# Kernel optimization log

Measured on AMD Instinct MI355X. Metric: run time of the kernel, lower is better.

The kernel has to match this reference:

```python
import jax, jax.numpy as jnp
import numpy as np

DIM = 128      # input node feature dim
GS = 64        # SAGEConv output dim
AF = 32        # additional (ir_score) feature dim
NB = 2         # nb_classes
G = 8192       # num_graphs in batch
NPG = 16       # nodes per graph
N = G * NPG    # total nodes = 131072
E = 2097152    # total edges (avg degree 16)


def setup_inputs() -> dict:
    key = jax.random.key(0)
    ks = jax.random.split(key, 10)

    def w(k, shape, fan_in):
        return jax.random.normal(k, shape, jnp.float32) / np.sqrt(fan_in)

    return {
        "x": jax.random.normal(ks[0], (N, DIM), jnp.float32),
        "edge_index": jax.random.randint(ks[1], (2, E), 0, N),
        "set_indices": jax.random.randint(ks[2], (G, 2), 0, NPG),
        "batch_ids": jnp.repeat(jnp.arange(G), NPG),  # sorted graph ids, PyG style
        "ir_score": jax.random.uniform(ks[3], (G, AF), jnp.float32),
        "W_l": w(ks[4], (DIM, GS), DIM),
        "b_l": jnp.zeros((GS,), jnp.float32),
        "W_r": w(ks[5], (DIM, GS), DIM),
        "W_ir": w(ks[6], (AF, 2 * GS), AF),
        "b_ir": jnp.zeros((2 * GS,), jnp.float32),
        "W1": w(ks[7], ((2 * GS) * (2 * GS), 200), (2 * GS) * (2 * GS)),
        "b1": jnp.zeros((200,), jnp.float32),
        "W2": w(ks[8], (200, NB), 200),
        "b2": jnp.zeros((NB,), jnp.float32),
    }


def reference(x, edge_index, set_indices, batch_ids, ir_score,
              W_l, b_l, W_r, W_ir, b_ir, W1, b1, W2, b2):
    n = x.shape[0]
    src, dst = edge_index[0], edge_index[1]

    # SAGEConv (mean aggregation): out = lin_l(mean_{j in N(i)} x_j) + lin_r(x_i)
    agg = jax.ops.segment_sum(x[src], dst, num_segments=n)           # [N, DIM]
    deg = jax.ops.segment_sum(jnp.ones((src.shape[0],), x.dtype), dst, num_segments=n)
    mean = agg / jnp.maximum(deg, 1.0)[:, None]
    h = jax.nn.relu(mean @ W_l + b_l + x @ W_r)                      # [N, GS]

    # per-graph node counts -> index bases (cumsum), then global pair indices
    g = set_indices.shape[0]
    num_nodes = jax.ops.segment_sum(jnp.ones((n,), jnp.float32), batch_ids, num_segments=g)
    csum = jnp.cumsum(num_nodes.astype(jnp.int64))
    index_bases = jnp.concatenate([jnp.zeros((1,), jnp.int64), csum[:-1]])
    sib = index_bases[:, None] + set_indices                         # [G, 2]

    pair = h[sib].reshape(g, 2 * GS)                                 # gather + flatten

    # fusion: relu(linear(ir_score)) then per-graph outer product
    S = jax.nn.relu(ir_score @ W_ir + b_ir)                          # [G, 2*GS]
    outer = jnp.einsum('gi,gj->gij', pair, S).reshape(g, -1)         # [G, (2GS)^2]

    # decode MLP
    z = jax.nn.relu(outer @ W1 + b1)                                 # [G, 200]
    logits = z @ W2 + b2                                             # [G, NB]
    return logits
```

## Files before the change

kernel.cpp:

```cpp
#include <hip/hip_runtime.h>

#define NN   131072
#define GG   8192
#define EE   2097152
#define KBIG 16384
#define NPAD 224
#define NSPLIT 8
#define NSEL  16384
#define SBUCK 256
#define SUBC  4
#define SCAPS 336
#define SCAPT (SUBC*SCAPS)

typedef _Float16 half_t;
typedef __attribute__((ext_vector_type(8))) _Float16 half8;
typedef __attribute__((ext_vector_type(4))) float floatx4;

__device__ inline floatx4 mfma16(half8 a, half8 b, floatx4 c) {
  return __builtin_amdgcn_mfma_f32_16x16x32_f16(a, b, c, 0, 0, 0);
}

__global__ void prep_w(const float* __restrict__ Wl, const float* __restrict__ Wr,
                       half_t* __restrict__ Wt) {
  int idx = blockIdx.x * blockDim.x + threadIdx.x;
  int n = idx >> 7, k = idx & 127;
  float v = (n < 64) ? Wl[k * 64 + n] : Wr[k * 64 + (n - 64)];
  Wt[n * 128 + k] = (half_t)v;
}
__global__ void prep_w1p(const float* __restrict__ W1, half_t* __restrict__ W1p) {
  int idx = blockIdx.x * blockDim.x + threadIdx.x;
  int lane = idx & 63;
  int t = idx >> 6;
  int nt = t % 14; t /= 14;
  int jj = t & 1;  t >>= 1;
  int i  = t & 15; t >>= 4;
  int ph = t & 1;  t >>= 1;
  int split = t;
  int n = nt * 16 + (lane & 15);
  int k0 = split * 2048 + i * 128 + ph * 64 + jj * 32 + (lane >> 4) * 8;
  half8 v;
#pragma unroll
  for (int e = 0; e < 8; e++)
    v[e] = (half_t)((n < 200) ? W1[(size_t)(k0 + e) * 200 + n] : 0.f);
  *(half8*)(W1p + (size_t)idx * 8) = v;
}

__global__ void set_slots(const int* __restrict__ set_idx, int* __restrict__ nodemap,
                          int* __restrict__ slot_node) {
  int idx = blockIdx.x * blockDim.x + threadIdx.x;
  int g = idx >> 1, which = idx & 1;
  int node = g * 16 + set_idx[g * 2 + which];
  slot_node[idx] = node;
  nodemap[node] = idx;
}

__global__ void filter_scatter(const int* __restrict__ src, const int* __restrict__ dst,
                               const int* __restrict__ nodemap,
                               int* __restrict__ scnt, unsigned int* __restrict__ sbuf) {
  int e = blockIdx.x * blockDim.x + threadIdx.x;
  int d = dst[e];
  int slot = nodemap[d];
  if (slot >= 0) {
    int b = slot >> 6;
    int sub = blockIdx.x & (SUBC - 1);
    int pos = atomicAdd(&scnt[(b * SUBC + sub) * 16], 1);
    if (pos < SCAPS)
      sbuf[(size_t)(b * SUBC + sub) * SCAPS + pos] =
          (unsigned int)src[e] | ((unsigned int)(slot & 63) << 17);
  }
}

__global__ __launch_bounds__(256) void y_gemm(const float* __restrict__ x,
                                              const half_t* __restrict__ WtG,
                                              half_t* __restrict__ y16) {
  __shared__ half_t wlds[64 * 128];
  __shared__ half_t ybuf[64 * 72];
  int tid = threadIdx.x, w = tid >> 6, lane = tid & 63;
  int m = lane & 15, q = lane >> 4, kc = q * 8;
#pragma unroll
  for (int it = 0; it < 4; it++) {
    int cb = (it * 4 + w) * 64;
    const half_t* g = WtG + ((size_t)cb + lane) * 8;
    half_t* l = wlds + (size_t)cb * 8;
    __builtin_amdgcn_global_load_lds((const __attribute__((address_space(1))) uint32_t*)g,
                                     (__attribute__((address_space(3))) uint32_t*)l, 16, 0, 0);
  }
  int node0 = blockIdx.x * 64 + w * 16;
  float4 xu[4][2];
#pragma unroll
  for (int step = 0; step < 4; step++) {
    const float* xp = x + (size_t)(node0 + m) * 128 + step * 32 + kc;
    xu[step][0] = *(const float4*)xp;
    xu[step][1] = *(const float4*)(xp + 4);
  }
  __syncthreads();
  floatx4 acc[4];
#pragma unroll
  for (int nt = 0; nt < 4; nt++) acc[nt] = (floatx4){0.f, 0.f, 0.f, 0.f};
#pragma unroll
  for (int step = 0; step < 4; step++) {
    float4 u0 = xu[step][0], u1 = xu[step][1];
    half8 av = {(half_t)u0.x, (half_t)u0.y, (half_t)u0.z, (half_t)u0.w,
                (half_t)u1.x, (half_t)u1.y, (half_t)u1.z, (half_t)u1.w};
    int k0 = step * 32 + kc;
#pragma unroll
    for (int nt = 0; nt < 4; nt++) {
      half8 bv = *(const half8*)(wlds + (nt * 16 + m) * 128 + k0);
      acc[nt] = mfma16(av, bv, acc[nt]);
    }
  }
#pragma unroll
  for (int nt = 0; nt < 4; nt++)
#pragma unroll
    for (int r = 0; r < 4; r++)
      ybuf[(w * 16 + q * 4 + r) * 72 + nt * 16 + m] = (half_t)acc[nt][r];
  __syncthreads();
#pragma unroll
  for (int c = tid; c < 512; c += 256) {
    int row = c >> 3, co = (c & 7) * 8;
    *(half8*)(y16 + (size_t)(blockIdx.x * 64 + row) * 64 + co) =
        *(const half8*)(ybuf + row * 72 + co);
  }
}

__global__ __launch_bounds__(256) void r_slots(const float* __restrict__ x,
                                               const half_t* __restrict__ WtG,
                                               const float* __restrict__ b_l,
                                               const int* __restrict__ slot_node,
                                               half_t* __restrict__ r_slot) {
  int tid = threadIdx.x, w = tid >> 6, lane = tid & 63;
  int m = lane & 15, q = lane >> 4, kc = q * 8;
  int s0 = blockIdx.x * 64 + w * 16;
  int node = slot_node[s0 + m];
  floatx4 acc[4];
#pragma unroll
  for (int nt = 0; nt < 4; nt++) acc[nt] = (floatx4){0.f, 0.f, 0.f, 0.f};
#pragma unroll
  for (int step = 0; step < 4; step++) {
    int k0 = step * 32 + kc;
    const float* xp = x + (size_t)node * 128 + k0;
    float4 u0 = *(const float4*)xp;
    float4 u1 = *(const float4*)(xp + 4);
    half8 av = {(half_t)u0.x, (half_t)u0.y, (half_t)u0.z, (half_t)u0.w,
                (half_t)u1.x, (half_t)u1.y, (half_t)u1.z, (half_t)u1.w};
#pragma unroll
    for (int nt = 0; nt < 4; nt++) {
      half8 bv = *(const half8*)(WtG + (size_t)(64 + nt * 16 + m) * 128 + k0);
      acc[nt] = mfma16(av, bv, acc[nt]);
    }
  }
#pragma unroll
  for (int nt = 0; nt < 4; nt++) {
    int n = nt * 16 + m;
    float bias = b_l[n];
#pragma unroll
    for (int r = 0; r < 4; r++) {
      int s = s0 + q * 4 + r;
      r_slot[(size_t)s * 64 + n] = (half_t)(acc[nt][r] + bias);
    }
  }
}

__global__ __launch_bounds__(256) void slot_agg(const unsigned int* __restrict__ sbuf,
                                                const int* __restrict__ scnt,
                                                const half_t* __restrict__ y16,
                                                const half_t* __restrict__ r_slot,
                                                half_t* __restrict__ h_slot) {
  __shared__ int sorted[SCAPT];
  __shared__ int hist[64];
  __shared__ int base[64];
  __shared__ int start[65];
  int b = blockIdx.x, tid = threadIdx.x;
  if (tid < 64) hist[tid] = 0;
  __syncthreads();
  unsigned int myedge[2 * SUBC];
  int mycnt = 0;
#pragma unroll
  for (int sub = 0; sub < SUBC; sub++) {
    int n = scnt[(b * SUBC + sub) * 16]; if (n > SCAPS) n = SCAPS;
    const unsigned int* eb = sbuf + (size_t)(b * SUBC + sub) * SCAPS;
    for (int e = tid; e < n; e += 256) {
      unsigned int pk = eb[e];
      myedge[mycnt++] = pk;
      atomicAdd(&hist[pk >> 17], 1);
    }
  }
  __syncthreads();
  if (tid < 64) {
    int v = hist[tid];
    int sum = v;
#pragma unroll
    for (int off = 1; off < 64; off <<= 1) {
      int u = __shfl_up(sum, off);
      if (tid >= off) sum += u;
    }
    start[tid] = sum - v;
    base[tid]  = sum - v;
    if (tid == 63) start[64] = sum;
  }
  __syncthreads();
  for (int i = 0; i < mycnt; i++) {
    unsigned int pk = myedge[i];
    int pos = atomicAdd(&base[pk >> 17], 1);
    sorted[pos] = (int)(pk & 0x1FFFF);
  }
  __syncthreads();
  int s = tid >> 2, p = tid & 3;
  int e0 = start[s], e1 = start[s + 1];
  float acc[16];
#pragma unroll
  for (int j = 0; j < 16; j++) acc[j] = 0.f;
  int e = e0;
  for (; e + 2 <= e1; e += 2) {
    int s0 = sorted[e], s1 = sorted[e + 1];
    const half8* p0 = (const half8*)(y16 + (size_t)s0 * 64 + p * 16);
    const half8* p1 = (const half8*)(y16 + (size_t)s1 * 64 + p * 16);
    half8 a0 = p0[0], c0 = p0[1], a1 = p1[0], c1 = p1[1];
#pragma unroll
    for (int j = 0; j < 8; j++) {
      acc[j]     += (float)a0[j] + (float)a1[j];
      acc[8 + j] += (float)c0[j] + (float)c1[j];
    }
  }
  if (e < e1) {
    int s0 = sorted[e];
    const half8* p0 = (const half8*)(y16 + (size_t)s0 * 64 + p * 16);
    half8 a0 = p0[0], c0 = p0[1];
#pragma unroll
    for (int j = 0; j < 8; j++) { acc[j] += (float)a0[j]; acc[8 + j] += (float)c0[j]; }
  }
  int slot = b * 64 + s;
  float inv = 1.0f / fmaxf((float)(e1 - e0), 1.0f);
  const half8* rr = (const half8*)(r_slot + (size_t)slot * 64 + p * 16);
  half8 r0 = rr[0], r1 = rr[1];
  half8 o0, o1;
#pragma unroll
  for (int j = 0; j < 8; j++) {
    o0[j] = (half_t)fmaxf(acc[j] * inv + (float)r0[j], 0.f);
    o1[j] = (half_t)fmaxf(acc[8 + j] * inv + (float)r1[j], 0.f);
  }
  half8* hp = (half8*)(h_slot + (size_t)slot * 64 + p * 16);
  hp[0] = o0;
  hp[1] = o1;
}

__global__ void s_pair_kernel(const float* __restrict__ ir, const float* __restrict__ W_ir,
                              const float* __restrict__ b_ir, half_t* __restrict__ S16,
                              const half_t* __restrict__ h_slot,
                              const int* __restrict__ nodemap,
                              const int* __restrict__ set_idx, half_t* __restrict__ pair16) {
  int idx = blockIdx.x * blockDim.x + threadIdx.x;
  int g = idx >> 7, o = idx & 127;
  const float* irow = ir + g * 32;
  float sv = b_ir[o];
#pragma unroll
  for (int a = 0; a < 32; a++) sv += irow[a] * W_ir[a * 128 + o];
  S16[idx] = (half_t)fmaxf(sv, 0.f);
  int which = o >> 6, c = o & 63;
  int node = g * 16 + set_idx[g * 2 + which];
  int slot = nodemap[node];
  pair16[idx] = h_slot[(size_t)slot * 64 + c];
}

__global__ __launch_bounds__(256, 2) void biggemm(const half_t* __restrict__ pair16,
                                                  const half_t* __restrict__ S16,
                                                  const half_t* __restrict__ W1p,
                                                  float* __restrict__ zpart) {
  __shared__ __align__(16) half_t bbuf[2][28 * 512];
  __shared__ half_t pls[16][128];
  int bx = blockIdx.x;
  int mt = bx >> 3, split = bx & 7;
  int g0 = mt * 128;
  int tid = threadIdx.x, w = tid >> 6, lane = tid & 63;
  int wm = w >> 1, wn = w & 1;
  int m = lane & 15, q = lane >> 4, kc = q * 8;
  int ntb = wn * 7;

  auto stage = [&](int s, int buf) {
#pragma unroll
    for (int ff = 0; ff < 7; ff++) {
      int f = ff * 4 + w;
      const half_t* gsrc = W1p + (((size_t)(split * 32 + s) * 28) + f) * 512 + lane * 8;
      half_t* ldst = &bbuf[buf][f * 512];
      __builtin_amdgcn_global_load_lds((const __attribute__((address_space(1))) uint32_t*)gsrc,
                                       (__attribute__((address_space(3))) uint32_t*)ldst, 16, 0, 0);
    }
  };

  {
    int row = tid & 127, sel = tid >> 7;
    half8 pa = *(const half8*)(pair16 + (size_t)(g0 + row) * 128 + split * 16 + sel * 8);
#pragma unroll
    for (int j = 0; j < 8; j++) pls[sel * 8 + j][row] = pa[j];
  }
  __syncthreads();

  stage(0, 0);
  stage(1, 1);

  floatx4 acc[4][7];
#pragma unroll
  for (int sb = 0; sb < 4; sb++)
#pragma unroll
    for (int t = 0; t < 7; t++) acc[sb][t] = (floatx4){0.f, 0.f, 0.f, 0.f};

  half8 sf[4][2];
#pragma unroll
  for (int ph = 0; ph < 2; ph++) {
#pragma unroll
    for (int sub = 0; sub < 4; sub++) {
      int grow = g0 + wm * 64 + sub * 16 + m;
#pragma unroll
      for (int j2 = 0; j2 < 2; j2++)
        sf[sub][j2] = *(const half8*)(S16 + (size_t)grow * 128 + ph * 64 + j2 * 32 + kc);
    }
#pragma unroll
    for (int i = 0; i < 16; i++) {
      const int s = ph * 16 + i;
      const int cur = s & 1;
      if (ph == 1 && i == 15) {
        asm volatile("s_waitcnt vmcnt(0)" ::: "memory");
      } else {
        asm volatile("s_waitcnt vmcnt(7)" ::: "memory");
      }
      __builtin_amdgcn_sched_barrier(0);
      __builtin_amdgcn_s_barrier();
      __builtin_amdgcn_sched_barrier(0);

      half_t p0 = pls[i][wm * 64 + 0 * 16 + m];
      half_t p1 = pls[i][wm * 64 + 1 * 16 + m];
      half_t p2 = pls[i][wm * 64 + 2 * 16 + m];
      half_t p3 = pls[i][wm * 64 + 3 * 16 + m];
      const half_t* bb = bbuf[cur];
#pragma unroll
      for (int jj = 0; jj < 2; jj++) {
        half8 a0 = sf[0][jj] * p0;
        half8 a1 = sf[1][jj] * p1;
        half8 a2 = sf[2][jj] * p2;
        half8 a3 = sf[3][jj] * p3;
#pragma unroll
        for (int t = 0; t < 7; t++) {
          half8 bv = *(const half8*)(bb + (jj * 14 + ntb + t) * 512 + lane * 8);
          acc[0][t] = mfma16(a0, bv, acc[0][t]);
          acc[1][t] = mfma16(a1, bv, acc[1][t]);
          acc[2][t] = mfma16(a2, bv, acc[2][t]);
          acc[3][t] = mfma16(a3, bv, acc[3][t]);
        }
      }

      if (s < 30) {
        __builtin_amdgcn_sched_barrier(0);
        __builtin_amdgcn_s_barrier();
        __builtin_amdgcn_sched_barrier(0);
        stage(s + 2, cur);
      }
    }
  }

#pragma unroll
  for (int sub = 0; sub < 4; sub++)
#pragma unroll
    for (int t = 0; t < 7; t++)
#pragma unroll
      for (int r = 0; r < 4; r++) {
        int row = g0 + wm * 64 + sub * 16 + q * 4 + r;
        zpart[((size_t)split * GG + row) * NPAD + (ntb + t) * 16 + m] = acc[sub][t][r];
      }
}

__global__ __launch_bounds__(256) void reduce_mlp(const float* __restrict__ zpart,
                                                  const float* __restrict__ b1,
                                                  const float* __restrict__ W2,
                                                  const float* __restrict__ b2,
                                                  float* __restrict__ out) {
  int tid = threadIdx.x;
  int w = tid >> 6, lane = tid & 63;
  int g = blockIdx.x * 4 + w;
  float p0 = 0.f, p1 = 0.f;
#pragma unroll
  for (int qq = 0; qq < 4; qq++) {
    int c = qq * 64 + lane;
    if (c < 200) {
      float z = 0.f;
#pragma unroll
      for (int sp = 0; sp < NSPLIT; sp++)
        z += zpart[((size_t)sp * GG + g) * NPAD + c];
      z += b1[c];
      z = fmaxf(z, 0.f);
      p0 += z * W2[c * 2];
      p1 += z * W2[c * 2 + 1];
    }
  }
#pragma unroll
  for (int off = 32; off; off >>= 1) {
    p0 += __shfl_down(p0, off);
    p1 += __shfl_down(p1, off);
  }
  if (lane == 0) {
    out[g * 2] = p0 + b2[0];
    out[g * 2 + 1] = p1 + b2[1];
  }
}

extern "C" void kernel_launch(void* const* d_in, const int* in_sizes, int n_in,
                              void* d_out, int out_size, void* d_ws, size_t ws_size,
                              hipStream_t stream) {
  const float* x     = (const float*)d_in[0];
  const int*   ei    = (const int*)d_in[1];
  const int*   setix = (const int*)d_in[2];
  const float* ir    = (const float*)d_in[4];
  const float* W_l   = (const float*)d_in[5];
  const float* b_l   = (const float*)d_in[6];
  const float* W_r   = (const float*)d_in[7];
  const float* W_ir  = (const float*)d_in[8];
  const float* b_ir  = (const float*)d_in[9];
  const float* W1    = (const float*)d_in[10];
  const float* b1    = (const float*)d_in[11];
  const float* W2    = (const float*)d_in[12];
  const float* b2    = (const float*)d_in[13];
  float* out = (float*)d_out;

  char* ws = (char*)d_ws;
  size_t off = 0;
  auto alloc = [&](size_t bytes) -> void* {
    void* p = ws + off;
    off = (off + bytes + 255) & ~(size_t)255;
    return p;
  };
  size_t pool_start = off;
  int* nodemap   = (int*)alloc((size_t)NN * 4);
  int* slot_node = (int*)alloc((size_t)NSEL * 4);
  int* scnt      = (int*)alloc((size_t)SBUCK * SUBC * 16 * 4);
  unsigned int* sbuf = (unsigned int*)alloc((size_t)SBUCK * SUBC * SCAPS * 4);
  half_t* y16    = (half_t*)alloc((size_t)NN * 64 * 2);
  half_t* r_slot = (half_t*)alloc((size_t)NSEL * 64 * 2);
  half_t* h_slot = (half_t*)alloc((size_t)NSEL * 64 * 2);
  float* zpart = (float*)(ws + pool_start);
  {
    size_t zend = pool_start + (((size_t)NSPLIT * GG * NPAD * 4 + 255) & ~(size_t)255);
    if (off < zend) off = zend;
  }
  half_t* Wt     = (half_t*)alloc(128 * 128 * 2);
  half_t* W1p    = (half_t*)alloc((size_t)NPAD * KBIG * 2);
  half_t* S16    = (half_t*)alloc((size_t)GG * 128 * 2);
  half_t* pair16 = (half_t*)alloc((size_t)GG * 128 * 2);
  (void)ws_size; (void)in_sizes; (void)n_in; (void)out_size;

  const int* esrc = ei;
  const int* edst = ei + EE;

  hipMemsetAsync(nodemap, 0xFF, (size_t)NN * 4, stream);
  hipMemsetAsync(scnt, 0, (size_t)SBUCK * SUBC * 16 * 4, stream);

  prep_w<<<(128 * 128) / 256, 256, 0, stream>>>(W_l, W_r, Wt);
  prep_w1p<<<(NPAD * KBIG / 8) / 256, 256, 0, stream>>>(W1, W1p);

  set_slots<<<NSEL / 256, 256, 0, stream>>>(setix, nodemap, slot_node);
  filter_scatter<<<EE / 256, 256, 0, stream>>>(esrc, edst, nodemap, scnt, sbuf);

  y_gemm<<<NN / 64, 256, 0, stream>>>(x, Wt, y16);
  r_slots<<<NSEL / 64, 256, 0, stream>>>(x, Wt, b_l, slot_node, r_slot);
  slot_agg<<<SBUCK, 256, 0, stream>>>(sbuf, scnt, y16, r_slot, h_slot);

  s_pair_kernel<<<(GG * 128) / 256, 256, 0, stream>>>(ir, W_ir, b_ir, S16, h_slot, nodemap, setix, pair16);

  biggemm<<<(GG / 128) * NSPLIT, 256, 0, stream>>>(pair16, S16, W1p, zpart);
  reduce_mlp<<<GG / 4, 256, 0, stream>>>(zpart, b1, W2, b2, out);
}
```

Measured before the change: 263.7 us.

## Fuse prep and mid kernels, replace nodemap lookup with direct set-index test

Merges the weight-prep, slot setup and counter clearing into one kernel, and the y GEMM, root GEMM and edge filtering into another, using block-index ranges to select the role. Drops the nodemap array and its memset by computing each edge's slot from dst's graph and local index compared against set_indices. This cuts launch and memset overhead and random nodemap reads, at the cost of more branchy kernels with shared LDS sizing and an assumption of 16 nodes per graph.

```diff
diff --git a/kernel.cpp b/kernel.cpp
--- a/kernel.cpp
+++ b/kernel.cpp
@@ -20,143 +20,152 @@
   return __builtin_amdgcn_mfma_f32_16x16x32_f16(a, b, c, 0, 0, 0);
 }
 
-__global__ void prep_w(const float* __restrict__ Wl, const float* __restrict__ Wr,
-                       half_t* __restrict__ Wt) {
-  int idx = blockIdx.x * blockDim.x + threadIdx.x;
-  int n = idx >> 7, k = idx & 127;
-  float v = (n < 64) ? Wl[k * 64 + n] : Wr[k * 64 + (n - 64)];
-  Wt[n * 128 + k] = (half_t)v;
-}
-__global__ void prep_w1p(const float* __restrict__ W1, half_t* __restrict__ W1p) {
-  int idx = blockIdx.x * blockDim.x + threadIdx.x;
-  int lane = idx & 63;
-  int t = idx >> 6;
-  int nt = t % 14; t /= 14;
-  int jj = t & 1;  t >>= 1;
-  int i  = t & 15; t >>= 4;
-  int ph = t & 1;  t >>= 1;
-  int split = t;
-  int n = nt * 16 + (lane & 15);
-  int k0 = split * 2048 + i * 128 + ph * 64 + jj * 32 + (lane >> 4) * 8;
-  half8 v;
-#pragma unroll
-  for (int e = 0; e < 8; e++)
-    v[e] = (half_t)((n < 200) ? W1[(size_t)(k0 + e) * 200 + n] : 0.f);
-  *(half8*)(W1p + (size_t)idx * 8) = v;
-}
-
-__global__ void set_slots(const int* __restrict__ set_idx, int* __restrict__ nodemap,
-                          int* __restrict__ slot_node) {
-  int idx = blockIdx.x * blockDim.x + threadIdx.x;
-  int g = idx >> 1, which = idx & 1;
-  int node = g * 16 + set_idx[g * 2 + which];
-  slot_node[idx] = node;
-  nodemap[node] = idx;
-}
-
-__global__ void filter_scatter(const int* __restrict__ src, const int* __restrict__ dst,
-                               const int* __restrict__ nodemap,
-                               int* __restrict__ scnt, unsigned int* __restrict__ sbuf) {
-  int e = blockIdx.x * blockDim.x + threadIdx.x;
-  int d = dst[e];
-  int slot = nodemap[d];
-  if (slot >= 0) {
-    int b = slot >> 6;
-    int sub = blockIdx.x & (SUBC - 1);
-    int pos = atomicAdd(&scnt[(b * SUBC + sub) * 16], 1);
-    if (pos < SCAPS)
-      sbuf[(size_t)(b * SUBC + sub) * SCAPS + pos] =
-          (unsigned int)src[e] | ((unsigned int)(slot & 63) << 17);
-  }
-}
-
-__global__ __launch_bounds__(256) void y_gemm(const float* __restrict__ x,
-                                              const half_t* __restrict__ WtG,
-                                              half_t* __restrict__ y16) {
+__global__ __launch_bounds__(256) void prep_all(const float* __restrict__ Wl,
+                                                const float* __restrict__ Wr,
+                                                const float* __restrict__ W1,
+                                                const int* __restrict__ setix,
+                                                half_t* __restrict__ Wt,
+                                                half_t* __restrict__ W1p,
+                                                int* __restrict__ slot_node,
+                                                int* __restrict__ scnt) {
+  int b = blockIdx.x, tid = threadIdx.x;
+  if (b < 1792) {
+    int idx = b * 256 + tid;
+    int lane = idx & 63;
+    int t = idx >> 6;
+    int nt = t % 14; t /= 14;
+    int jj = t & 1;  t >>= 1;
+    int i  = t & 15; t >>= 4;
+    int ph = t & 1;  t >>= 1;
+    int split = t;
+    int n = nt * 16 + (lane & 15);
+    int k0 = split * 2048 + i * 128 + ph * 64 + jj * 32 + (lane >> 4) * 8;
+    half8 v;
+#pragma unroll
+    for (int e = 0; e < 8; e++)
+      v[e] = (half_t)((n < 200) ? W1[(size_t)(k0 + e) * 200 + n] : 0.f);
+    *(half8*)(W1p + (size_t)idx * 8) = v;
+  } else if (b < 1856) {
+    int idx = (b - 1792) * 256 + tid;
+    int n = idx >> 7, k = idx & 127;
+    float v = (n < 64) ? Wl[k * 64 + n] : Wr[k * 64 + (n - 64)];
+    Wt[n * 128 + k] = (half_t)v;
+  } else if (b < 1920) {
+    int idx = (b - 1856) * 256 + tid;
+    slot_node[idx] = (idx >> 1) * 16 + setix[idx];
+  } else {
+    int idx = (b - 1920) * 256 + tid;
+    scnt[idx] = 0;
+  }
+}
+
+__global__ __launch_bounds__(256) void fused_mid(const float* __restrict__ x,
+                                                 const half_t* __restrict__ WtG,
+                                                 const float* __restrict__ b_l,
+                                                 const int* __restrict__ slot_node,
+                                                 const int* __restrict__ setix,
+                                                 const int* __restrict__ src,
+                                                 const int* __restrict__ dst,
+                                                 int* __restrict__ scnt,
+                                                 unsigned int* __restrict__ sbuf,
+                                                 half_t* __restrict__ y16,
+                                                 half_t* __restrict__ r_slot) {
   __shared__ half_t wlds[64 * 128];
   __shared__ half_t ybuf[64 * 72];
-  int tid = threadIdx.x, w = tid >> 6, lane = tid & 63;
-  int m = lane & 15, q = lane >> 4, kc = q * 8;
-#pragma unroll
-  for (int it = 0; it < 4; it++) {
-    int cb = (it * 4 + w) * 64;
-    const half_t* g = WtG + ((size_t)cb + lane) * 8;
-    half_t* l = wlds + (size_t)cb * 8;
-    __builtin_amdgcn_global_load_lds((const __attribute__((address_space(1))) uint32_t*)g,
-                                     (__attribute__((address_space(3))) uint32_t*)l, 16, 0, 0);
-  }
-  int node0 = blockIdx.x * 64 + w * 16;
-  float4 xu[4][2];
-#pragma unroll
-  for (int step = 0; step < 4; step++) {
-    const float* xp = x + (size_t)(node0 + m) * 128 + step * 32 + kc;
-    xu[step][0] = *(const float4*)xp;
-    xu[step][1] = *(const float4*)(xp + 4);
-  }
-  __syncthreads();
-  floatx4 acc[4];
-#pragma unroll
-  for (int nt = 0; nt < 4; nt++) acc[nt] = (floatx4){0.f, 0.f, 0.f, 0.f};
-#pragma unroll
-  for (int step = 0; step < 4; step++) {
-    float4 u0 = xu[step][0], u1 = xu[step][1];
-    half8 av = {(half_t)u0.x, (half_t)u0.y, (half_t)u0.z, (half_t)u0.w,
-                (half_t)u1.x, (half_t)u1.y, (half_t)u1.z, (half_t)u1.w};
-    int k0 = step * 32 + kc;
+  int b = blockIdx.x, tid = threadIdx.x;
+  if (b < 2048) {
+    int w = tid >> 6, lane = tid & 63;
+    int m = lane & 15, q = lane >> 4, kc = q * 8;
+#pragma unroll
+    for (int it = 0; it < 4; it++) {
+      int cb = (it * 4 + w) * 64;
+      const half_t* g = WtG + ((size_t)cb + lane) * 8;
+      half_t* l = wlds + (size_t)cb * 8;
+      __builtin_amdgcn_global_load_lds((const __attribute__((address_space(1))) uint32_t*)g,
+                                       (__attribute__((address_space(3))) uint32_t*)l, 16, 0, 0);
+    }
+    int node0 = b * 64 + w * 16;
+    float4 xu[4][2];
+#pragma unroll
+    for (int step = 0; step < 4; step++) {
+      const float* xp = x + (size_t)(node0 + m) * 128 + step * 32 + kc;
+      xu[step][0] = *(const float4*)xp;
+      xu[step][1] = *(const float4*)(xp + 4);
+    }
+    __syncthreads();
+    floatx4 acc[4];
+#pragma unroll
+    for (int nt = 0; nt < 4; nt++) acc[nt] = (floatx4){0.f, 0.f, 0.f, 0.f};
+#pragma unroll
+    for (int step = 0; step < 4; step++) {
+      float4 u0 = xu[step][0], u1 = xu[step][1];
+      half8 av = {(half_t)u0.x, (half_t)u0.y, (half_t)u0.z, (half_t)u0.w,
+                  (half_t)u1.x, (half_t)u1.y, (half_t)u1.z, (half_t)u1.w};
+      int k0 = step * 32 + kc;
+#pragma unroll
+      for (int nt = 0; nt < 4; nt++) {
+        half8 bv = *(const half8*)(wlds + (nt * 16 + m) * 128 + k0);
+        acc[nt] = mfma16(av, bv, acc[nt]);
+      }
+    }
+#pragma unroll
+    for (int nt = 0; nt < 4; nt++)
+#pragma unroll
+      for (int r = 0; r < 4; r++)
+        ybuf[(w * 16 + q * 4 + r) * 72 + nt * 16 + m] = (half_t)acc[nt][r];
+    __syncthreads();
+#pragma unroll
+    for (int c = tid; c < 512; c += 256) {
+      int row = c >> 3, co = (c & 7) * 8;
+      *(half8*)(y16 + (size_t)(b * 64 + row) * 64 + co) =
+          *(const half8*)(ybuf + row * 72 + co);
+    }
+  } else if (b < 2304) {
+    int w = tid >> 6, lane = tid & 63;
+    int m = lane & 15, q = lane >> 4, kc = q * 8;
+    int s0 = (b - 2048) * 64 + w * 16;
+    int node = slot_node[s0 + m];
+    floatx4 acc[4];
+#pragma unroll
+    for (int nt = 0; nt < 4; nt++) acc[nt] = (floatx4){0.f, 0.f, 0.f, 0.f};
+#pragma unroll
+    for (int step = 0; step < 4; step++) {
+      int k0 = step * 32 + kc;
+      const float* xp = x + (size_t)node * 128 + k0;
+      float4 u0 = *(const float4*)xp;
+      float4 u1 = *(const float4*)(xp + 4);
+      half8 av = {(half_t)u0.x, (half_t)u0.y, (half_t)u0.z, (half_t)u0.w,
+                  (half_t)u1.x, (half_t)u1.y, (half_t)u1.z, (half_t)u1.w};
+#pragma unroll
+      for (int nt = 0; nt < 4; nt++) {
+        half8 bv = *(const half8*)(WtG + (size_t)(64 + nt * 16 + m) * 128 + k0);
+        acc[nt] = mfma16(av, bv, acc[nt]);
+      }
+    }
 #pragma unroll
     for (int nt = 0; nt < 4; nt++) {
-      half8 bv = *(const half8*)(wlds + (nt * 16 + m) * 128 + k0);
-      acc[nt] = mfma16(av, bv, acc[nt]);
-    }
-  }
-#pragma unroll
-  for (int nt = 0; nt < 4; nt++)
-#pragma unroll
-    for (int r = 0; r < 4; r++)
-      ybuf[(w * 16 + q * 4 + r) * 72 + nt * 16 + m] = (half_t)acc[nt][r];
-  __syncthreads();
-#pragma unroll
-  for (int c = tid; c < 512; c += 256) {
-    int row = c >> 3, co = (c & 7) * 8;
-    *(half8*)(y16 + (size_t)(blockIdx.x * 64 + row) * 64 + co) =
-        *(const half8*)(ybuf + row * 72 + co);
-  }
-}
-
-__global__ __launch_bounds__(256) void r_slots(const float* __restrict__ x,
-                                               const half_t* __restrict__ WtG,
-                                               const float* __restrict__ b_l,
-                                               const int* __restrict__ slot_node,
-                                               half_t* __restrict__ r_slot) {
-  int tid = threadIdx.x, w = tid >> 6, lane = tid & 63;
-  int m = lane & 15, q = lane >> 4, kc = q * 8;
-  int s0 = blockIdx.x * 64 + w * 16;
-  int node = slot_node[s0 + m];
-  floatx4 acc[4];
-#pragma unroll
-  for (int nt = 0; nt < 4; nt++) acc[nt] = (floatx4){0.f, 0.f, 0.f, 0.f};
-#pragma unroll
-  for (int step = 0; step < 4; step++) {
-    int k0 = step * 32 + kc;
-    const float* xp = x + (size_t)node * 128 + k0;
-    float4 u0 = *(const float4*)xp;
-    float4 u1 = *(const float4*)(xp + 4);
-    half8 av = {(half_t)u0.x, (half_t)u0.y, (half_t)u0.z, (half_t)u0.w,
-                (half_t)u1.x, (half_t)u1.y, (half_t)u1.z, (half_t)u1.w};
-#pragma unroll
-    for (int nt = 0; nt < 4; nt++) {
-      half8 bv = *(const half8*)(WtG + (size_t)(64 + nt * 16 + m) * 128 + k0);
-      acc[nt] = mfma16(av, bv, acc[nt]);
-    }
-  }
-#pragma unroll
-  for (int nt = 0; nt < 4; nt++) {
-    int n = nt * 16 + m;
-    float bias = b_l[n];
-#pragma unroll
-    for (int r = 0; r < 4; r++) {
-      int s = s0 + q * 4 + r;
-      r_slot[(size_t)s * 64 + n] = (half_t)(acc[nt][r] + bias);
+      int n = nt * 16 + m;
+      float bias = b_l[n];
+#pragma unroll
+      for (int r = 0; r < 4; r++) {
+        int s = s0 + q * 4 + r;
+        r_slot[(size_t)s * 64 + n] = (half_t)(acc[nt][r] + bias);
+      }
+    }
+  } else {
+    int eb = b - 2304;
+    int e = eb * 256 + tid;
+    int d = dst[e];
+    int g = d >> 4, local = d & 15;
+    int si0 = setix[g * 2], si1 = setix[g * 2 + 1];
+    int slot = (local == si0) ? g * 2 : ((local == si1) ? g * 2 + 1 : -1);
+    if (slot >= 0) {
+      int bk = slot >> 6;
+      int sub = eb & (SUBC - 1);
+      int pos = atomicAdd(&scnt[(bk * SUBC + sub) * 16], 1);
+      if (pos < SCAPS)
+        sbuf[(size_t)(bk * SUBC + sub) * SCAPS + pos] =
+            (unsigned int)src[e] | ((unsigned int)(slot & 63) << 17);
     }
   }
 }
@@ -247,7 +256,6 @@
 __global__ void s_pair_kernel(const float* __restrict__ ir, const float* __restrict__ W_ir,
                               const float* __restrict__ b_ir, half_t* __restrict__ S16,
                               const half_t* __restrict__ h_slot,
-                              const int* __restrict__ nodemap,
                               const int* __restrict__ set_idx, half_t* __restrict__ pair16) {
   int idx = blockIdx.x * blockDim.x + threadIdx.x;
   int g = idx >> 7, o = idx & 127;
@@ -257,8 +265,8 @@
   for (int a = 0; a < 32; a++) sv += irow[a] * W_ir[a * 128 + o];
   S16[idx] = (half_t)fmaxf(sv, 0.f);
   int which = o >> 6, c = o & 63;
-  int node = g * 16 + set_idx[g * 2 + which];
-  int slot = nodemap[node];
+  int li = set_idx[g * 2 + which];
+  int slot = (li == set_idx[g * 2]) ? g * 2 : g * 2 + 1;
   pair16[idx] = h_slot[(size_t)slot * 64 + c];
 }
 
@@ -428,7 +436,6 @@
     return p;
   };
   size_t pool_start = off;
-  int* nodemap   = (int*)alloc((size_t)NN * 4);
   int* slot_node = (int*)alloc((size_t)NSEL * 4);
   int* scnt      = (int*)alloc((size_t)SBUCK * SUBC * 16 * 4);
   unsigned int* sbuf = (unsigned int*)alloc((size_t)SBUCK * SUBC * SCAPS * 4);
@@ -449,21 +456,11 @@
   const int* esrc = ei;
   const int* edst = ei + EE;
 
-  hipMemsetAsync(nodemap, 0xFF, (size_t)NN * 4, stream);
-  hipMemsetAsync(scnt, 0, (size_t)SBUCK * SUBC * 16 * 4, stream);
-
-  prep_w<<<(128 * 128) / 256, 256, 0, stream>>>(W_l, W_r, Wt);
-  prep_w1p<<<(NPAD * KBIG / 8) / 256, 256, 0, stream>>>(W1, W1p);
-
-  set_slots<<<NSEL / 256, 256, 0, stream>>>(setix, nodemap, slot_node);
-  filter_scatter<<<EE / 256, 256, 0, stream>>>(esrc, edst, nodemap, scnt, sbuf);
-
-  y_gemm<<<NN / 64, 256, 0, stream>>>(x, Wt, y16);
-  r_slots<<<NSEL / 64, 256, 0, stream>>>(x, Wt, b_l, slot_node, r_slot);
+  prep_all<<<1984, 256, 0, stream>>>(W_l, W_r, W1, setix, Wt, W1p, slot_node, scnt);
+  fused_mid<<<10496, 256, 0, stream>>>(x, Wt, b_l, slot_node, setix, esrc, edst,
+                                       scnt, sbuf, y16, r_slot);
   slot_agg<<<SBUCK, 256, 0, stream>>>(sbuf, scnt, y16, r_slot, h_slot);
-
-  s_pair_kernel<<<(GG * 128) / 256, 256, 0, stream>>>(ir, W_ir, b_ir, S16, h_slot, nodemap, setix, pair16);
-
+  s_pair_kernel<<<(GG * 128) / 256, 256, 0, stream>>>(ir, W_ir, b_ir, S16, h_slot, setix, pair16);
   biggemm<<<(GG / 128) * NSPLIT, 256, 0, stream>>>(pair16, S16, W1p, zpart);
   reduce_mlp<<<GG / 4, 256, 0, stream>>>(zpart, b1, W2, b2, out);
 }
```

Result: faster. 256.2 us (-2.8%).
